# Kernel optimization log

Hardware: AMD Instinct MI355X
Metric: run time of the kernel (lower is better)

Reference implementation:

```python
import jax, jax.numpy as jnp
import numpy as np

BS = 4
EMBED = 256
HEADS = 8
LEVELS = 4
POINTS = 4
HD = EMBED // HEADS  # 32
SHAPES = np.array([[96, 96], [48, 48], [24, 24], [12, 12]], dtype=np.int64)
LQ = int((SHAPES[:, 0] * SHAPES[:, 1]).sum())  # 12240


def _offset_bias():
    # faithful to MSDeformableAttention._reset_parameters grid init
    thetas = np.arange(HEADS, dtype=np.float32) * (2.0 * np.pi / HEADS)
    g = np.stack([np.cos(thetas), np.sin(thetas)], -1)
    g = g / np.abs(g).max(-1, keepdims=True)
    g = np.tile(g.reshape(HEADS, 1, 1, 2), (1, LEVELS, POINTS, 1))
    g = g * np.arange(1, POINTS + 1, dtype=np.float32).reshape(1, 1, -1, 1)
    return jnp.asarray(g.reshape(-1), dtype=jnp.float32)


def setup_inputs() -> dict:
    key = jax.random.key(0)
    ks = jax.random.split(key, 8)
    tp = HEADS * LEVELS * POINTS
    d = {}
    d["query"] = jax.random.normal(ks[0], (BS, LQ, EMBED), jnp.float32)
    d["reference_points"] = jax.random.uniform(ks[1], (BS, LQ, LEVELS, 2), jnp.float32)
    d["value"] = jax.random.normal(ks[2], (BS, LQ, EMBED), jnp.float32)
    d["value_spatial_shapes"] = SHAPES  # static numpy, int
    d["W_off"] = jax.random.normal(ks[3], (EMBED, tp * 2), jnp.float32) * 0.01
    d["b_off"] = _offset_bias()
    d["W_attn"] = jax.random.normal(ks[4], (EMBED, tp), jnp.float32) * 0.02
    d["b_attn"] = jnp.zeros((tp,), jnp.float32)
    d["W_val"] = jax.random.normal(ks[5], (EMBED, EMBED), jnp.float32) * (1.0 / np.sqrt(EMBED).astype(np.float32))
    d["b_val"] = jnp.zeros((EMBED,), jnp.float32)
    d["W_out"] = jax.random.normal(ks[6], (EMBED, EMBED), jnp.float32) * (1.0 / np.sqrt(EMBED).astype(np.float32))
    d["b_out"] = jnp.zeros((EMBED,), jnp.float32)
    return d


def _bilinear_sample(img, grid):
    # img: [B,H,W,C]; grid: [B,Q,P,2] in [-1,1] (x,y)
    # matches F.grid_sample(mode='bilinear', padding_mode='zeros', align_corners=False)
    B, H, W, C = img.shape
    gx = (grid[..., 0] + 1.0) * (W * 0.5) - 0.5
    gy = (grid[..., 1] + 1.0) * (H * 0.5) - 0.5
    x0 = jnp.floor(gx)
    y0 = jnp.floor(gy)
    wx = gx - x0
    wy = gy - y0
    x0i = x0.astype(jnp.int32)
    y0i = y0.astype(jnp.int32)
    x1i = x0i + 1
    y1i = y0i + 1
    flat = img.reshape(B, H * W, C)

    def corner(xi, yi, w):
        valid = (xi >= 0) & (xi < W) & (yi >= 0) & (yi < H)
        idx = jnp.clip(yi, 0, H - 1) * W + jnp.clip(xi, 0, W - 1)
        v = jnp.take_along_axis(flat, idx.reshape(B, -1, 1), axis=1)
        v = v.reshape(idx.shape + (C,))
        return v * (w * valid)[..., None]

    return (corner(x0i, y0i, (1.0 - wx) * (1.0 - wy))
            + corner(x1i, y0i, wx * (1.0 - wy))
            + corner(x0i, y1i, (1.0 - wx) * wy)
            + corner(x1i, y1i, wx * wy))


def reference(query, reference_points, value, value_spatial_shapes,
              W_off, b_off, W_attn, b_attn, W_val, b_val, W_out, b_out):
    shapes = np.asarray(value_spatial_shapes)  # static [L,2] (H,W)
    bs, Lq, _ = query.shape
    v = (value @ W_val + b_val).reshape(bs, -1, HEADS, HD)  # [bs,Lv,H,hd]
    off = (query @ W_off + b_off).reshape(bs, Lq, HEADS, LEVELS, POINTS, 2)
    aw = jax.nn.softmax((query @ W_attn + b_attn).reshape(bs, Lq, HEADS, LEVELS * POINTS), axis=-1)
    aw = aw.reshape(bs, Lq, HEADS, LEVELS, POINTS)
    # normalizer is (W,H) per level
    norm = jnp.asarray(shapes[:, ::-1].copy(), jnp.float32).reshape(1, 1, 1, LEVELS, 1, 2)
    loc = reference_points[:, :, None, :, None, :] + off / norm
    grids = 2.0 * loc - 1.0  # [bs,Lq,H,L,P,2]

    acc = jnp.zeros((bs * HEADS, Lq, HD), query.dtype)
    start = 0
    for lvl in range(LEVELS):
        h, w = int(shapes[lvl, 0]), int(shapes[lvl, 1])
        v_l = v[:, start:start + h * w].reshape(bs, h, w, HEADS, HD)
        v_l = v_l.transpose(0, 3, 1, 2, 4).reshape(bs * HEADS, h, w, HD)
        g_l = grids[:, :, :, lvl].transpose(0, 2, 1, 3, 4).reshape(bs * HEADS, Lq, POINTS, 2)
        s_l = _bilinear_sample(v_l, g_l)  # [bs*H, Lq, P, hd]
        w_l = aw[:, :, :, lvl].transpose(0, 2, 1, 3).reshape(bs * HEADS, Lq, POINTS)
        acc = acc + jnp.einsum('bqpc,bqp->bqc', s_l, w_l)
        start += h * w

    out = acc.reshape(bs, HEADS, Lq, HD).transpose(0, 2, 1, 3).reshape(bs, Lq, EMBED)
    return out @ W_out + b_out
```

## Files before the change

### kernel.cpp

```cpp
#include <hip/hip_runtime.h>
#include <hip/hip_bf16.h>

static constexpr int BS     = 4;
static constexpr int EMBED  = 256;
static constexpr int HEADS  = 8;
static constexpr int LEVELS = 4;
static constexpr int POINTS = 4;
static constexpr int HD     = 32;
static constexpr int LQ     = 12240;
static constexpr int NROW   = BS * LQ;
static constexpr int LVL_W[4]  = {96, 48, 24, 12};
static constexpr int LVL_H[4]  = {96, 48, 24, 12};
static constexpr int LVL_ST[4] = {0, 9216, 11520, 12096};

typedef __attribute__((ext_vector_type(8))) short short8;
typedef __attribute__((ext_vector_type(4))) float f32x4;

__device__ __forceinline__ unsigned short f2bf(float f) {
    unsigned int u = __float_as_uint(f);
    unsigned int r = (u + 0x7FFFu + ((u >> 16) & 1u)) >> 16;
    return (unsigned short)r;
}
__device__ __forceinline__ float bf2f(unsigned short b) {
    return __uint_as_float(((unsigned int)b) << 16);
}

__global__ __launch_bounds__(256) void prep_weights(
    const float* __restrict__ W_off, const float* __restrict__ W_attn,
    const float* __restrict__ W_val, const float* __restrict__ W_out,
    unsigned short* __restrict__ WT_oa, unsigned short* __restrict__ WT_val,
    unsigned short* __restrict__ WT_out)
{
    const int gid = blockIdx.x * 256 + threadIdx.x;
    const int k = gid & 255;
    const int n = gid >> 8;
    if (n < 384) {
        const float v = (n < 256) ? W_off[k * 256 + n] : W_attn[k * 128 + (n - 256)];
        WT_oa[n * 256 + k] = f2bf(v);
    } else if (n < 640) {
        const int nn = n - 384;
        WT_val[nn * 256 + k] = f2bf(W_val[k * 256 + nn]);
    } else {
        const int nn = n - 640;
        WT_out[nn * 256 + k] = f2bf(W_out[k * 256 + nn]);
    }
}

template <int NTW, bool A_BF16, bool OUT_BF16>
__global__ __launch_bounds__(256) void gemm_mfma(
    const void* __restrict__ Av, const unsigned short* __restrict__ Wt,
    const float* __restrict__ bias0, const float* __restrict__ bias1, int nsplit,
    void* __restrict__ Cv, int N)
{
    constexpr int NB = NTW * 64;
    constexpr int K  = 256;
    __shared__ __align__(16) unsigned short As[64][40];
    __shared__ __align__(16) unsigned short Bs[NB][40];

    const int tid = threadIdx.x;
    const int m0 = blockIdx.y * 64;
    const int n0 = blockIdx.x * NB;
    const int w  = tid >> 6;
    const int l  = tid & 63;
    const int lm = l & 15;
    const int lq = l >> 4;

    const int sr = tid >> 2;
    const int kg = (tid & 3) * 8;

    float4 pa0, pa1; short8 pa_bf;
    short8 pb[NTW];

    auto gload = [&](int k0) {
        if (A_BF16) {
            const unsigned short* A = (const unsigned short*)Av;
            pa_bf = *(const short8*)&A[(size_t)(m0 + sr) * K + k0 + kg];
        } else {
            const float* A = (const float*)Av;
            const float* ap = &A[(size_t)(m0 + sr) * K + k0 + kg];
            pa0 = *(const float4*)ap;
            pa1 = *(const float4*)(ap + 4);
        }
        #pragma unroll
        for (int i = 0; i < NTW; ++i) {
            const int slot = tid + i * 256;
            const int n  = slot >> 2;
            const int kk = (slot & 3) * 8;
            pb[i] = *(const short8*)&Wt[(size_t)(n0 + n) * K + k0 + kk];
        }
    };

    f32x4 acc[4][NTW];
    #pragma unroll
    for (int rg = 0; rg < 4; ++rg)
        #pragma unroll
        for (int nt = 0; nt < NTW; ++nt)
            acc[rg][nt] = (f32x4){0.f, 0.f, 0.f, 0.f};

    gload(0);
    #pragma unroll 2
    for (int k0 = 0; k0 < K; k0 += 32) {
        if (A_BF16) {
            *(short8*)&As[sr][kg] = pa_bf;
        } else {
            uint4 pk;
            pk.x = (unsigned int)f2bf(pa0.x) | ((unsigned int)f2bf(pa0.y) << 16);
            pk.y = (unsigned int)f2bf(pa0.z) | ((unsigned int)f2bf(pa0.w) << 16);
            pk.z = (unsigned int)f2bf(pa1.x) | ((unsigned int)f2bf(pa1.y) << 16);
            pk.w = (unsigned int)f2bf(pa1.z) | ((unsigned int)f2bf(pa1.w) << 16);
            *(uint4*)&As[sr][kg] = pk;
        }
        #pragma unroll
        for (int i = 0; i < NTW; ++i) {
            const int slot = tid + i * 256;
            const int n  = slot >> 2;
            const int kk = (slot & 3) * 8;
            *(short8*)&Bs[n][kk] = pb[i];
        }
        __syncthreads();

        if (k0 + 32 < K) gload(k0 + 32);

        short8 af[4];
        #pragma unroll
        for (int rg = 0; rg < 4; ++rg)
            af[rg] = *(const short8*)&As[rg * 16 + lm][lq * 8];
        #pragma unroll
        for (int nt = 0; nt < NTW; ++nt) {
            const short8 bf = *(const short8*)&Bs[(w * NTW + nt) * 16 + lm][lq * 8];
            #pragma unroll
            for (int rg = 0; rg < 4; ++rg)
                acc[rg][nt] = __builtin_amdgcn_mfma_f32_16x16x32_bf16(af[rg], bf, acc[rg][nt], 0, 0, 0);
        }
        __syncthreads();
    }

    #pragma unroll
    for (int nt = 0; nt < NTW; ++nt) {
        const int col = n0 + (w * NTW + nt) * 16 + lm;
        const float b = (col < nsplit) ? bias0[col] : bias1[col - nsplit];
        #pragma unroll
        for (int rg = 0; rg < 4; ++rg)
            #pragma unroll
            for (int r = 0; r < 4; ++r) {
                const int row = m0 + rg * 16 + lq * 4 + r;
                const float v = acc[rg][nt][r] + b;
                if (OUT_BF16) ((unsigned short*)Cv)[(size_t)row * N + col] = f2bf(v);
                else          ((float*)Cv)[(size_t)row * N + col] = v;
            }
    }
}

__global__ __launch_bounds__(256) void loc_aw_kernel(
    float* __restrict__ OA, const float* __restrict__ refp)
{
    const int tid = threadIdx.x;
    const int row = blockIdx.x * 2 + (tid >> 7);
    const int t = tid & 127;
    const int l = (t >> 2) & 3;
    float* rowp = OA + (size_t)row * 384;

    float logit = rowp[256 + t];
    float m = logit;
    #pragma unroll
    for (int d = 8; d >= 1; d >>= 1) m = fmaxf(m, __shfl_xor(m, d, 16));
    float e = __expf(logit - m);
    float s = e;
    #pragma unroll
    for (int d = 8; d >= 1; d >>= 1) s += __shfl_xor(s, d, 16);
    rowp[256 + t] = e / s;

    const float ox = rowp[t * 2 + 0];
    const float oy = rowp[t * 2 + 1];
    const float rx = refp[(size_t)row * 8 + l * 2 + 0];
    const float ry = refp[(size_t)row * 8 + l * 2 + 1];
    const float Wl = (float)LVL_W[l];
    const float Hl = (float)LVL_H[l];
    const float lx = rx + ox / Wl;
    const float ly = ry + oy / Hl;
    rowp[t * 2 + 0] = lx * Wl - 0.5f;
    rowp[t * 2 + 1] = ly * Hl - 0.5f;
}

__global__ __launch_bounds__(256) void sample_kernel(
    const unsigned short* __restrict__ V,
    const float* __restrict__ OA,
    unsigned short* __restrict__ ACC)
{
    __shared__ float oas[2][384];
    __shared__ float red[2][64][4];

    const int tid = threadIdx.x;
    const int w   = tid >> 6;
    const int r2  = w >> 1;
    const int lg  = w & 1;
    const int l64 = tid & 63;
    const int h   = l64 >> 3;
    const int c4  = (l64 & 7) * 4;
    const int row = blockIdx.x * 2 + r2;
    const int b   = row / LQ;

    if (tid < 192) {
        const int r = tid / 96;
        const int c = (tid % 96) * 4;
        *(float4*)&oas[r][c] =
            *(const float4*)&OA[(size_t)(blockIdx.x * 2 + r) * 384 + c];
    }
    __syncthreads();

    const unsigned short* vb = V + ((size_t)b * LQ * EMBED + h * HD + c4);

    float acc[4] = {0.f, 0.f, 0.f, 0.f};
    ushort4 dat[2][8];
    float   cw[2][8];

    auto prep = [&](int pp, int buf) {
        const int l = 2 * lg + (pp >> 1);
        const int Wl = LVL_W[l], Hl = LVL_H[l], st = LVL_ST[l];
        #pragma unroll
        for (int j = 0; j < 2; ++j) {
            const int p  = (pp & 1) * 2 + j;
            const int lp = l * 4 + p;
            const float gx  = oas[r2][h * 32 + lp * 2 + 0];
            const float gy  = oas[r2][h * 32 + lp * 2 + 1];
            const float wgt = oas[r2][256 + h * 16 + lp];

            const float fx = floorf(gx), fy = floorf(gy);
            const float wx = gx - fx,    wy = gy - fy;
            const int x0 = (int)fx, y0 = (int)fy;
            const int x1 = x0 + 1,  y1 = y0 + 1;

            const bool bx0 = ((unsigned)x0 < (unsigned)Wl);
            const bool bx1 = ((unsigned)x1 < (unsigned)Wl);
            const bool by0 = ((unsigned)y0 < (unsigned)Hl);
            const bool by1 = ((unsigned)y1 < (unsigned)Hl);
            cw[buf][j * 4 + 0] = (bx0 && by0) ? (1.f - wx) * (1.f - wy) * wgt : 0.f;
            cw[buf][j * 4 + 1] = (bx1 && by0) ? wx * (1.f - wy) * wgt : 0.f;
            cw[buf][j * 4 + 2] = (bx0 && by1) ? (1.f - wx) * wy * wgt : 0.f;
            cw[buf][j * 4 + 3] = (bx1 && by1) ? wx * wy * wgt : 0.f;

            const int cx0 = min(max(x0, 0), Wl - 1);
            const int cx1 = min(max(x1, 0), Wl - 1);
            const int cy0 = min(max(y0, 0), Hl - 1);
            const int cy1 = min(max(y1, 0), Hl - 1);
            dat[buf][j * 4 + 0] = *(const ushort4*)(vb + (size_t)(st + cy0 * Wl + cx0) * EMBED);
            dat[buf][j * 4 + 1] = *(const ushort4*)(vb + (size_t)(st + cy0 * Wl + cx1) * EMBED);
            dat[buf][j * 4 + 2] = *(const ushort4*)(vb + (size_t)(st + cy1 * Wl + cx0) * EMBED);
            dat[buf][j * 4 + 3] = *(const ushort4*)(vb + (size_t)(st + cy1 * Wl + cx1) * EMBED);
        }
    };
    auto consume = [&](int buf) {
        #pragma unroll
        for (int k = 0; k < 8; ++k) {
            const float wk = cw[buf][k];
            acc[0] = fmaf(wk, bf2f(dat[buf][k].x), acc[0]);
            acc[1] = fmaf(wk, bf2f(dat[buf][k].y), acc[1]);
            acc[2] = fmaf(wk, bf2f(dat[buf][k].z), acc[2]);
            acc[3] = fmaf(wk, bf2f(dat[buf][k].w), acc[3]);
        }
    };

    prep(0, 0);
    #pragma unroll
    for (int pp = 0; pp < 4; ++pp) {
        if (pp < 3) prep(pp + 1, (pp + 1) & 1);
        consume(pp & 1);
    }

    if (lg == 1) {
        red[r2][l64][0] = acc[0]; red[r2][l64][1] = acc[1];
        red[r2][l64][2] = acc[2]; red[r2][l64][3] = acc[3];
    }
    __syncthreads();
    if (lg == 0) {
        ushort4 o;
        o.x = f2bf(acc[0] + red[r2][l64][0]);
        o.y = f2bf(acc[1] + red[r2][l64][1]);
        o.z = f2bf(acc[2] + red[r2][l64][2]);
        o.w = f2bf(acc[3] + red[r2][l64][3]);
        *(ushort4*)(ACC + (size_t)row * EMBED + h * HD + c4) = o;
    }
}

extern "C" void kernel_launch(void* const* d_in, const int* in_sizes, int n_in,
                              void* d_out, int out_size, void* d_ws, size_t ws_size,
                              hipStream_t stream) {
    const float* query  = (const float*)d_in[0];
    const float* refp   = (const float*)d_in[1];
    const float* value  = (const float*)d_in[2];
    const float* W_off  = (const float*)d_in[4];
    const float* b_off  = (const float*)d_in[5];
    const float* W_attn = (const float*)d_in[6];
    const float* b_attn = (const float*)d_in[7];
    const float* W_val  = (const float*)d_in[8];
    const float* b_val  = (const float*)d_in[9];
    const float* W_out  = (const float*)d_in[10];
    const float* b_out  = (const float*)d_in[11];
    float* out = (float*)d_out;

    unsigned short* WT_oa  = (unsigned short*)d_ws;
    unsigned short* WT_val = WT_oa  + 384 * 256;
    unsigned short* WT_out = WT_val + 256 * 256;
    unsigned short* V      = WT_out + 256 * 256;
    float*          OA     = (float*)(V + (size_t)NROW * EMBED);
    unsigned short* ACCb   = (unsigned short*)(OA + (size_t)NROW * 384);

    dim3 blk(256);

    prep_weights<<<896, blk, 0, stream>>>(W_off, W_attn, W_val, W_out,
                                          WT_oa, WT_val, WT_out);
    gemm_mfma<4, false, true><<<dim3(1, NROW / 64), blk, 0, stream>>>(
        value, WT_val, b_val, b_val, 256, V, 256);
    gemm_mfma<3, false, false><<<dim3(2, NROW / 64), blk, 0, stream>>>(
        query, WT_oa, b_off, b_attn, 256, OA, 384);
    loc_aw_kernel<<<NROW / 2, blk, 0, stream>>>(OA, refp);
    sample_kernel<<<NROW / 2, blk, 0, stream>>>(V, OA, ACCb);
    gemm_mfma<4, true, false><<<dim3(1, NROW / 64), blk, 0, stream>>>(
        ACCb, WT_out, b_out, b_out, 256, out, 256);
}
```

Baseline: 378.7 us.

## Restructure deformable sampling: precompute corner offsets/weights in LDS, 16B gathers, packed FMA

The sampling kernel now handles four query rows per block. A cooperative pre-pass computes the bilinear corner offsets and weights for all 512 (row, head, level, point) samples and stores them in shared memory, so the main loop no longer recomputes them per lane. Each lane then gathers 16-byte chunks (8 bf16 channels) instead of 8 bytes and accumulates with v_pk_fma_f32 on packed float pairs. The two half-waves are combined with a cross-lane shuffle instead of an LDS reduction and second barrier. The cost is a larger LDS footprint (24 KB per block) and inline assembly that ties the code to this ISA.

```diff
diff --git a/kernel.cpp b/kernel.cpp
--- a/kernel.cpp
+++ b/kernel.cpp
@@ -15,6 +15,7 @@
 
 typedef __attribute__((ext_vector_type(8))) short short8;
 typedef __attribute__((ext_vector_type(4))) float f32x4;
+typedef __attribute__((ext_vector_type(2))) float f32x2;
 
 __device__ __forceinline__ unsigned short f2bf(float f) {
     unsigned int u = __float_as_uint(f);
@@ -23,6 +24,13 @@
 }
 __device__ __forceinline__ float bf2f(unsigned short b) {
     return __uint_as_float(((unsigned int)b) << 16);
+}
+
+__device__ __forceinline__ void pkfma(f32x2& a, unsigned int u, f32x2 w) {
+    f32x2 v;
+    v.x = __uint_as_float(u << 16);
+    v.y = __uint_as_float(u & 0xffff0000u);
+    asm("v_pk_fma_f32 %0, %1, %2, %0" : "+v"(a) : "v"(v), "v"(w));
 }
 
 __global__ __launch_bounds__(256) void prep_weights(
@@ -187,98 +195,127 @@
     const float* __restrict__ OA,
     unsigned short* __restrict__ ACC)
 {
-    __shared__ float oas[2][384];
-    __shared__ float red[2][64][4];
+    __shared__ unsigned int pr[512 * 12];
 
     const int tid = threadIdx.x;
-    const int w   = tid >> 6;
-    const int r2  = w >> 1;
-    const int lg  = w & 1;
-    const int l64 = tid & 63;
-    const int h   = l64 >> 3;
-    const int c4  = (l64 & 7) * 4;
-    const int row = blockIdx.x * 2 + r2;
-    const int b   = row / LQ;
-
-    if (tid < 192) {
-        const int r = tid / 96;
-        const int c = (tid % 96) * 4;
-        *(float4*)&oas[r][c] =
-            *(const float4*)&OA[(size_t)(blockIdx.x * 2 + r) * 384 + c];
+
+    #pragma unroll
+    for (int ss = 0; ss < 2; ++ss) {
+        const int s  = tid + ss * 256;
+        const int lp = s >> 5;
+        const int r  = (s >> 3) & 3;
+        const int h  = s & 7;
+        const int lvl = lp >> 2;
+        const int Wl = LVL_W[lvl], Hl = LVL_H[lvl], st = LVL_ST[lvl];
+        const float* rowp = OA + (size_t)(blockIdx.x * 4 + r) * 384;
+
+        const float gx  = rowp[h * 32 + lp * 2 + 0];
+        const float gy  = rowp[h * 32 + lp * 2 + 1];
+        const float wgt = rowp[256 + h * 16 + lp];
+
+        const float fx = floorf(gx), fy = floorf(gy);
+        const float wx = gx - fx,    wy = gy - fy;
+        const int x0 = (int)fx, y0 = (int)fy;
+        const int x1 = x0 + 1,  y1 = y0 + 1;
+
+        const bool bx0 = ((unsigned)x0 < (unsigned)Wl);
+        const bool bx1 = ((unsigned)x1 < (unsigned)Wl);
+        const bool by0 = ((unsigned)y0 < (unsigned)Hl);
+        const bool by1 = ((unsigned)y1 < (unsigned)Hl);
+        const float w00 = (bx0 && by0) ? (1.f - wx) * (1.f - wy) * wgt : 0.f;
+        const float w10 = (bx1 && by0) ? wx * (1.f - wy) * wgt : 0.f;
+        const float w01 = (bx0 && by1) ? (1.f - wx) * wy * wgt : 0.f;
+        const float w11 = (bx1 && by1) ? wx * wy * wgt : 0.f;
+
+        const int cx0 = min(max(x0, 0), Wl - 1);
+        const int cx1 = min(max(x1, 0), Wl - 1);
+        const int cy0 = min(max(y0, 0), Hl - 1);
+        const int cy1 = min(max(y1, 0), Hl - 1);
+
+        unsigned int* p = &pr[s * 12];
+        uint4 o;
+        o.x = (unsigned int)(st + cy0 * Wl + cx0) * 512u;
+        o.y = (unsigned int)(st + cy0 * Wl + cx1) * 512u;
+        o.z = (unsigned int)(st + cy1 * Wl + cx0) * 512u;
+        o.w = (unsigned int)(st + cy1 * Wl + cx1) * 512u;
+        *(uint4*)p = o;
+        uint4 wA, wB;
+        wA.x = __float_as_uint(w00); wA.y = wA.x;
+        wA.z = __float_as_uint(w10); wA.w = wA.z;
+        wB.x = __float_as_uint(w01); wB.y = wB.x;
+        wB.z = __float_as_uint(w11); wB.w = wB.z;
+        *(uint4*)(p + 4) = wA;
+        *(uint4*)(p + 8) = wB;
     }
     __syncthreads();
 
-    const unsigned short* vb = V + ((size_t)b * LQ * EMBED + h * HD + c4);
-
-    float acc[4] = {0.f, 0.f, 0.f, 0.f};
-    ushort4 dat[2][8];
-    float   cw[2][8];
-
-    auto prep = [&](int pp, int buf) {
-        const int l = 2 * lg + (pp >> 1);
-        const int Wl = LVL_W[l], Hl = LVL_H[l], st = LVL_ST[l];
-        #pragma unroll
-        for (int j = 0; j < 2; ++j) {
-            const int p  = (pp & 1) * 2 + j;
-            const int lp = l * 4 + p;
-            const float gx  = oas[r2][h * 32 + lp * 2 + 0];
-            const float gy  = oas[r2][h * 32 + lp * 2 + 1];
-            const float wgt = oas[r2][256 + h * 16 + lp];
-
-            const float fx = floorf(gx), fy = floorf(gy);
-            const float wx = gx - fx,    wy = gy - fy;
-            const int x0 = (int)fx, y0 = (int)fy;
-            const int x1 = x0 + 1,  y1 = y0 + 1;
-
-            const bool bx0 = ((unsigned)x0 < (unsigned)Wl);
-            const bool bx1 = ((unsigned)x1 < (unsigned)Wl);
-            const bool by0 = ((unsigned)y0 < (unsigned)Hl);
-            const bool by1 = ((unsigned)y1 < (unsigned)Hl);
-            cw[buf][j * 4 + 0] = (bx0 && by0) ? (1.f - wx) * (1.f - wy) * wgt : 0.f;
-            cw[buf][j * 4 + 1] = (bx1 && by0) ? wx * (1.f - wy) * wgt : 0.f;
-            cw[buf][j * 4 + 2] = (bx0 && by1) ? (1.f - wx) * wy * wgt : 0.f;
-            cw[buf][j * 4 + 3] = (bx1 && by1) ? wx * wy * wgt : 0.f;
-
-            const int cx0 = min(max(x0, 0), Wl - 1);
-            const int cx1 = min(max(x1, 0), Wl - 1);
-            const int cy0 = min(max(y0, 0), Hl - 1);
-            const int cy1 = min(max(y1, 0), Hl - 1);
-            dat[buf][j * 4 + 0] = *(const ushort4*)(vb + (size_t)(st + cy0 * Wl + cx0) * EMBED);
-            dat[buf][j * 4 + 1] = *(const ushort4*)(vb + (size_t)(st + cy0 * Wl + cx1) * EMBED);
-            dat[buf][j * 4 + 2] = *(const ushort4*)(vb + (size_t)(st + cy1 * Wl + cx0) * EMBED);
-            dat[buf][j * 4 + 3] = *(const ushort4*)(vb + (size_t)(st + cy1 * Wl + cx1) * EMBED);
-        }
+    const int w    = tid >> 6;
+    const int l    = tid & 63;
+    const int half = l >> 5;
+    const int head = (l >> 2) & 7;
+    const int c16  = (l & 3) * 16;
+
+    const int row  = __builtin_amdgcn_readfirstlane(blockIdx.x * 4 + w);
+    const int b    = row / LQ;
+    const char* vrow = (const char*)V + (size_t)b * ((size_t)LQ * 512);
+    const unsigned int lane_byte = (unsigned int)(head * 64 + c16);
+    const int sid0 = half * 8 * 32 + w * 8 + head;
+
+    unsigned int ofs[2][4];
+    f32x2 wp[2][4];
+    uint4 dat[2][4];
+    f32x2 acc[4];
+    #pragma unroll
+    for (int i = 0; i < 4; ++i) acc[i] = (f32x2){0.f, 0.f};
+
+    auto ldprep = [&](int j, int buf) {
+        const unsigned int* p = &pr[(sid0 + j * 32) * 12];
+        const uint4 o = *(const uint4*)p;
+        ofs[buf][0] = o.x; ofs[buf][1] = o.y; ofs[buf][2] = o.z; ofs[buf][3] = o.w;
+        #pragma unroll
+        for (int c = 0; c < 4; ++c)
+            wp[buf][c] = *(const f32x2*)(p + 4 + 2 * c);
+    };
+    auto ldval = [&](int buf) {
+        #pragma unroll
+        for (int c = 0; c < 4; ++c)
+            dat[buf][c] = *(const uint4*)(vrow + (lane_byte + ofs[buf][c]));
     };
     auto consume = [&](int buf) {
         #pragma unroll
-        for (int k = 0; k < 8; ++k) {
-            const float wk = cw[buf][k];
-            acc[0] = fmaf(wk, bf2f(dat[buf][k].x), acc[0]);
-            acc[1] = fmaf(wk, bf2f(dat[buf][k].y), acc[1]);
-            acc[2] = fmaf(wk, bf2f(dat[buf][k].z), acc[2]);
-            acc[3] = fmaf(wk, bf2f(dat[buf][k].w), acc[3]);
+        for (int c = 0; c < 4; ++c) {
+            const uint4 d = dat[buf][c];
+            const f32x2 ww = wp[buf][c];
+            pkfma(acc[0], d.x, ww);
+            pkfma(acc[1], d.y, ww);
+            pkfma(acc[2], d.z, ww);
+            pkfma(acc[3], d.w, ww);
         }
     };
 
-    prep(0, 0);
-    #pragma unroll
-    for (int pp = 0; pp < 4; ++pp) {
-        if (pp < 3) prep(pp + 1, (pp + 1) & 1);
-        consume(pp & 1);
-    }
-
-    if (lg == 1) {
-        red[r2][l64][0] = acc[0]; red[r2][l64][1] = acc[1];
-        red[r2][l64][2] = acc[2]; red[r2][l64][3] = acc[3];
-    }
-    __syncthreads();
-    if (lg == 0) {
-        ushort4 o;
-        o.x = f2bf(acc[0] + red[r2][l64][0]);
-        o.y = f2bf(acc[1] + red[r2][l64][1]);
-        o.z = f2bf(acc[2] + red[r2][l64][2]);
-        o.w = f2bf(acc[3] + red[r2][l64][3]);
-        *(ushort4*)(ACC + (size_t)row * EMBED + h * HD + c4) = o;
+    ldprep(0, 0);
+    ldval(0);
+    #pragma unroll
+    for (int j = 0; j < 8; ++j) {
+        if (j < 7) {
+            ldprep(j + 1, (j + 1) & 1);
+            ldval((j + 1) & 1);
+        }
+        consume(j & 1);
+    }
+
+    #pragma unroll
+    for (int i = 0; i < 4; ++i) {
+        acc[i].x += __shfl_xor(acc[i].x, 32);
+        acc[i].y += __shfl_xor(acc[i].y, 32);
+    }
+    if (half == 0) {
+        uint4 o;
+        o.x = (unsigned int)f2bf(acc[0].x) | ((unsigned int)f2bf(acc[0].y) << 16);
+        o.y = (unsigned int)f2bf(acc[1].x) | ((unsigned int)f2bf(acc[1].y) << 16);
+        o.z = (unsigned int)f2bf(acc[2].x) | ((unsigned int)f2bf(acc[2].y) << 16);
+        o.w = (unsigned int)f2bf(acc[3].x) | ((unsigned int)f2bf(acc[3].y) << 16);
+        *(uint4*)((char*)(ACC + (size_t)row * EMBED) + head * 64 + c16) = o;
     }
 }
 
@@ -314,7 +351,7 @@
     gemm_mfma<3, false, false><<<dim3(2, NROW / 64), blk, 0, stream>>>(
         query, WT_oa, b_off, b_attn, 256, OA, 384);
     loc_aw_kernel<<<NROW / 2, blk, 0, stream>>>(OA, refp);
-    sample_kernel<<<NROW / 2, blk, 0, stream>>>(V, OA, ACCb);
+    sample_kernel<<<NROW / 4, blk, 0, stream>>>(V, OA, ACCb);
     gemm_mfma<4, true, false><<<dim3(1, NROW / 64), blk, 0, stream>>>(
         ACCb, WT_out, b_out, b_out, 256, out, 256);
 }
```

New measurement: 382.9 us. No clear change (+1.1%).
